# Kernel tuning notes

Hardware: AMD Instinct MI355X
Metric: run time of the kernel (lower is better)

Reference implementation:

```python
import jax, jax.numpy as jnp
import numpy as np

N, E, F, DE, G, C = 50000, 800000, 64, 32, 512, 2
EPS = 1e-5


def setup_inputs() -> dict:
    key = jax.random.key(0)
    ks = jax.random.split(key, 12)
    Z = 2 * F + DE  # CGConv concat dim [x_i, x_j, edge_attr]
    inp = {
        "x": jax.random.normal(ks[0], (N, F), dtype=jnp.float32),
        "edge_index": jax.random.randint(ks[1], (2, E), 0, N, dtype=jnp.int32),
        "edge_attr": jax.random.normal(ks[2], (E, DE), dtype=jnp.float32),
        "batch": jnp.sort(jax.random.randint(ks[3], (N,), 0, G, dtype=jnp.int32)),
        # CGConv lin_f / lin_s : (2F+De) -> F, with bias
        "Wf": jax.random.normal(ks[4], (Z, F), dtype=jnp.float32) * 0.05,
        "bf": jnp.zeros((F,), dtype=jnp.float32),
        "Ws": jax.random.normal(ks[5], (Z, F), dtype=jnp.float32) * 0.05,
        "bs": jnp.zeros((F,), dtype=jnp.float32),
        # CGConv internal BatchNorm (training-mode batch stats)
        "bn_w": jnp.ones((F,), dtype=jnp.float32),
        "bn_b": jnp.zeros((F,), dtype=jnp.float32),
        # PyG LayerNorm (graph mode, batch=None -> whole-tensor stats)
        "ln_w": jnp.ones((F,), dtype=jnp.float32),
        "ln_b": jnp.zeros((F,), dtype=jnp.float32),
        # final linear (2F -> C) and output LayerNorm
        "Wl": jax.random.normal(ks[6], (2 * F, C), dtype=jnp.float32) * 0.05,
        "bl": jnp.zeros((C,), dtype=jnp.float32),
        "ln4_w": jnp.ones((C,), dtype=jnp.float32),
        "ln4_b": jnp.zeros((C,), dtype=jnp.float32),
    }
    return inp


def _pyg_layernorm(x, w, b):
    # torch_geometric.nn.LayerNorm, mode='graph', batch=None: whole-tensor stats
    xc = x - jnp.mean(x)
    out = xc / (jnp.sqrt(jnp.mean(xc * xc)) + EPS)
    return out * w + b


def reference(x, edge_index, edge_attr, batch, Wf, bf, Ws, bs, bn_w, bn_b,
              ln_w, ln_b, Wl, bl, ln4_w, ln4_b):
    src = edge_index[0]  # x_j (source)
    dst = edge_index[1]  # x_i (target / aggregation index)

    # CGConv message: sigmoid(lin_f(z)) * softplus(lin_s(z)), z=[x_i,x_j,e]
    z = jnp.concatenate([x[dst], x[src], edge_attr], axis=1)  # [E, 2F+De]
    msg = jax.nn.sigmoid(z @ Wf + bf) * jax.nn.softplus(z @ Ws + bs)  # [E,F]

    # scatter-add aggregation to target nodes
    agg = jax.ops.segment_sum(msg, dst, num_segments=N)  # [N,F]

    # CGConv batch_norm=True (training-mode batch statistics over nodes)
    mu = jnp.mean(agg, axis=0)
    var = jnp.mean((agg - mu) ** 2, axis=0)
    agg = (agg - mu) / jnp.sqrt(var + EPS) * bn_w + bn_b

    # residual
    h = agg + x

    # LayerNorm + softplus
    h = jax.nn.softplus(_pyg_layernorm(h, ln_w, ln_b))

    # global mean / add pooling over graphs
    add_pool = jax.ops.segment_sum(h, batch, num_segments=G)  # [G,F]
    counts = jax.ops.segment_sum(jnp.ones((N,), h.dtype), batch, num_segments=G)
    mean_pool = add_pool / jnp.maximum(counts, 1.0)[:, None]

    g = jnp.concatenate([mean_pool, add_pool], axis=1)  # [G, 2F]
    out = g @ Wl + bl  # [G, C]
    out = _pyg_layernorm(out, ln4_w, ln4_b)
    return out
```

## Files before the change

### kernel.cpp

```cpp
#include <hip/hip_runtime.h>
#include <math.h>

#define EPSF 1e-5f

typedef short bf16x8 __attribute__((ext_vector_type(8)));
typedef float f32x4 __attribute__((ext_vector_type(4)));

static __device__ __forceinline__ unsigned short f2bf(float x) {
  unsigned u = __float_as_uint(x);
  unsigned r = (u + 0x7FFFu + ((u >> 16) & 1u)) >> 16;
  return (unsigned short)r;
}

static __device__ __forceinline__ float msgv(float F, float S) {
  float sig = __builtin_amdgcn_rcpf(1.0f + __expf(-F));
  float sp = fmaxf(S, 0.f) + __logf(1.0f + __expf(-fabsf(S)));
  return sig * sp;
}

__global__ __launch_bounds__(256) void prep_kernel(
    const float* __restrict__ x, const float* __restrict__ Wf,
    const float* __restrict__ Ws, const int* __restrict__ ei,
    unsigned short* __restrict__ xbf, unsigned short* __restrict__ Bfrag,
    unsigned short* __restrict__ Bfrag2, int* __restrict__ deg, int NCV,
    int total8, int E) {
  const int b = blockIdx.x, t = threadIdx.x;
  if (b < NCV) {
    int i = b * 256 + t;
    if (i < total8) {
      float4 a = ((const float4*)x)[i * 2];
      float4 c = ((const float4*)x)[i * 2 + 1];
      unsigned short o[8];
      o[0] = f2bf(a.x); o[1] = f2bf(a.y); o[2] = f2bf(a.z); o[3] = f2bf(a.w);
      o[4] = f2bf(c.x); o[5] = f2bf(c.y); o[6] = f2bf(c.z); o[7] = f2bf(c.w);
      ((uint4*)xbf)[i] = *(uint4*)o;
    }
  } else if (b < NCV + 6) {
    int g2 = (b - NCV) * 256 + t;
    if (g2 < 1536) {
      const int ks = g2 >> 9, t8 = (g2 >> 6) & 7, l = g2 & 63;
      const int q = l & 15, g = l >> 4;
      const float* W = (t8 < 4) ? Wf : Ws;
      const int col = (t8 & 3) * 16 + q;
      unsigned short out[8];
#pragma unroll
      for (int i = 0; i < 8; ++i) {
        int kk = ks * 32 + g * 8 + i;
        int wr = (kk < 32) ? (128 + kk) : (32 + kk);
        out[i] = f2bf(W[(size_t)wr * 64 + col]);
      }
      *(uint4*)&Bfrag[((size_t)(ks * 8 + t8) * 64 + l) * 8] = *(uint4*)out;
    }
  } else if (b < NCV + 10) {
    int g2 = (b - NCV - 6) * 256 + t;
    if (g2 < 1024) {
      const int ks = g2 >> 9, t8 = (g2 >> 6) & 7, l = g2 & 63;
      const int q = l & 15, g = l >> 4;
      const float* W = (t8 < 4) ? Wf : Ws;
      const int col = (t8 & 3) * 16 + q;
      unsigned short out[8];
#pragma unroll
      for (int i = 0; i < 8; ++i) {
        int kk = ks * 32 + g * 8 + i;
        out[i] = f2bf(W[(size_t)kk * 64 + col]);
      }
      *(uint4*)&Bfrag2[((size_t)(ks * 8 + t8) * 64 + l) * 8] = *(uint4*)out;
    }
  } else {
    int i = (b - NCV - 10) * 256 + t;
    if (i < E) atomicAdd(&deg[ei[E + i]], 1);
  }
}

__global__ __launch_bounds__(256, 4) void node_mfma(
    const unsigned short* __restrict__ xbf,
    const unsigned short* __restrict__ Bfrag2, const float* __restrict__ bf_,
    const float* __restrict__ bs_, unsigned* __restrict__ Pd, int N) {
  __shared__ __align__(16) short Bsh[16][64][8];
  for (int i = threadIdx.x; i < 1024; i += 256)
    ((uint4*)Bsh)[i] = ((const uint4*)Bfrag2)[i];
  __syncthreads();
  const int lane = threadIdx.x & 63, w = threadIdx.x >> 6;
  const int q = lane & 15, g = lane >> 4;
  const int row0 = blockIdx.x * 64;
  const float bfv = bf_[w * 16 + q], bsv = bs_[w * 16 + q];
  f32x4 accf[4], accs[4];
#pragma unroll
  for (int mt = 0; mt < 4; ++mt) {
    accf[mt] = (f32x4){0.f, 0.f, 0.f, 0.f};
    accs[mt] = (f32x4){0.f, 0.f, 0.f, 0.f};
  }
#pragma unroll
  for (int ks = 0; ks < 2; ++ks) {
    const bf16x8 Bfr = *(const bf16x8*)&Bsh[ks * 8 + w][lane][0];
    const bf16x8 Bsr = *(const bf16x8*)&Bsh[ks * 8 + 4 + w][lane][0];
#pragma unroll
    for (int mt = 0; mt < 4; ++mt) {
      int row = min(row0 + mt * 16 + q, N - 1);
      const bf16x8 a = *(const bf16x8*)(xbf + (size_t)row * 64 + ks * 32 + g * 8);
      accf[mt] = __builtin_amdgcn_mfma_f32_16x16x32_bf16(a, Bfr, accf[mt], 0, 0, 0);
      accs[mt] = __builtin_amdgcn_mfma_f32_16x16x32_bf16(a, Bsr, accs[mt], 0, 0, 0);
    }
  }
#pragma unroll
  for (int mt = 0; mt < 4; ++mt) {
#pragma unroll
    for (int r = 0; r < 4; ++r) {
      int row = row0 + mt * 16 + g * 4 + r;
      if (row < N) {
        unsigned u = ((unsigned)f2bf(accf[mt][r] + bfv) << 16) |
                     (unsigned)f2bf(accs[mt][r] + bsv);
        Pd[(size_t)row * 64 + w * 16 + q] = u;
      }
    }
  }
}

__global__ __launch_bounds__(256) void scan_a(const int* __restrict__ deg,
                                              int* __restrict__ bsum, int N) {
  const int idx = blockIdx.x * 256 + threadIdx.x;
  int v = (idx < N) ? deg[idx] : 0;
#pragma unroll
  for (int o = 32; o > 0; o >>= 1) v += __shfl_down(v, o);
  __shared__ int ws4[4];
  if ((threadIdx.x & 63) == 0) ws4[threadIdx.x >> 6] = v;
  __syncthreads();
  if (threadIdx.x == 0) bsum[blockIdx.x] = ws4[0] + ws4[1] + ws4[2] + ws4[3];
}

__global__ __launch_bounds__(256) void scan_b(const int* __restrict__ bsum,
                                              int* __restrict__ bpre, int NB) {
  const int t = threadIdx.x;
  const int lane = t & 63, w = t >> 6;
  int v = (t < NB) ? bsum[t] : 0;
  int sc = v;
#pragma unroll
  for (int o = 1; o < 64; o <<= 1) {
    int u = __shfl_up(sc, o);
    if (lane >= o) sc += u;
  }
  __shared__ int wsum[4];
  if (lane == 63) wsum[w] = sc;
  __syncthreads();
  int add = 0;
#pragma unroll
  for (int k = 0; k < 4; ++k) add += (k < w) ? wsum[k] : 0;
  bpre[t] = (sc - v) + add;
}

__global__ __launch_bounds__(256) void scan_c(const int* __restrict__ deg,
                                              const int* __restrict__ bpre,
                                              int* __restrict__ cursor, int N) {
  const int t = threadIdx.x;
  const int lane = t & 63, w = t >> 6;
  const int idx = blockIdx.x * 256 + t;
  int d = (idx < N) ? deg[idx] : 0;
  int sc = d;
#pragma unroll
  for (int o = 1; o < 64; o <<= 1) {
    int u = __shfl_up(sc, o);
    if (lane >= o) sc += u;
  }
  __shared__ int wsum[4];
  if (lane == 63) wsum[w] = sc;
  __syncthreads();
  int add = bpre[blockIdx.x];
#pragma unroll
  for (int k = 0; k < 4; ++k) add += (k < w) ? wsum[k] : 0;
  if (idx < N) cursor[idx] = add + (sc - d);
}

__global__ void scatter_kernel(const int* __restrict__ ei,
                               int* __restrict__ cursor,
                               int4* __restrict__ epair4, int E) {
  int i = blockIdx.x * 256 + threadIdx.x;
  if (i >= E) return;
  int dst = ei[E + i];
  int pos = atomicAdd(&cursor[dst], 1);
  epair4[pos] = make_int4(i, ei[i], dst, 0);
}

__global__ __launch_bounds__(256, 4) void edge_fused(
    const int4* __restrict__ epair4, const float* __restrict__ eattr,
    const unsigned short* __restrict__ xbf,
    const unsigned short* __restrict__ Bfrag, const unsigned* __restrict__ Pd,
    float* __restrict__ agg, int T16, int N, int E) {
  __shared__ __align__(16) short Bsh[24][64][8];
  for (int i = threadIdx.x; i < 1536; i += 256)
    ((uint4*)Bsh)[i] = ((const uint4*)Bfrag)[i];
  __syncthreads();

  const int lane = threadIdx.x & 63, w = threadIdx.x >> 6;
  const int q = lane & 15, g = lane >> 4;

  const int nB = gridDim.x;
  const int cb = (blockIdx.x & 7) * (nB >> 3) + (blockIdx.x >> 3);
  const int q8 = T16 / nB, r8 = T16 - q8 * nB;
  const int t0 = cb * q8 + min(cb, r8);
  const int t1 = t0 + q8 + (cb < r8 ? 1 : 0);

  int t = t0 + w;
  if (t >= t1) return;

  int4 p = epair4[(size_t)t * 16 + q];
  unsigned exi = min((unsigned)p.x, (unsigned)(E - 1));
  float4 eA = *(const float4*)(eattr + (size_t)exi * 32 + g * 8);
  float4 eB = *(const float4*)(eattr + (size_t)exi * 32 + g * 8 + 4);
  unsigned su = min((unsigned)p.y, (unsigned)(N - 1));
  bf16x8 aX0 = *(const bf16x8*)(xbf + (size_t)su * 64 + g * 8);
  bf16x8 aX1 = *(const bf16x8*)(xbf + (size_t)su * 64 + 32 + g * 8);

  while (true) {
    const int tn = t + 4;
    const bool more = (tn < t1);
    int4 pn = p;
    float4 eAn = eA, eBn = eB;
    bf16x8 aX0n = aX0, aX1n = aX1;
    if (more) {
      pn = epair4[(size_t)tn * 16 + q];
      unsigned exn = min((unsigned)pn.x, (unsigned)(E - 1));
      eAn = *(const float4*)(eattr + (size_t)exn * 32 + g * 8);
      eBn = *(const float4*)(eattr + (size_t)exn * 32 + g * 8 + 4);
      unsigned sn = min((unsigned)pn.y, (unsigned)(N - 1));
      aX0n = *(const bf16x8*)(xbf + (size_t)sn * 64 + g * 8);
      aX1n = *(const bf16x8*)(xbf + (size_t)sn * 64 + 32 + g * 8);
    }

    bf16x8 aE;
    aE[0] = (short)f2bf(eA.x); aE[1] = (short)f2bf(eA.y);
    aE[2] = (short)f2bf(eA.z); aE[3] = (short)f2bf(eA.w);
    aE[4] = (short)f2bf(eB.x); aE[5] = (short)f2bf(eB.y);
    aE[6] = (short)f2bf(eB.z); aE[7] = (short)f2bf(eB.w);

    f32x4 accf[4], accs[4];
#pragma unroll
    for (int nt = 0; nt < 4; ++nt) {
      f32x4 z = {0.f, 0.f, 0.f, 0.f};
      accf[nt] = __builtin_amdgcn_mfma_f32_16x16x32_bf16(
          aE, *(const bf16x8*)&Bsh[nt][lane][0], z, 0, 0, 0);
      accf[nt] = __builtin_amdgcn_mfma_f32_16x16x32_bf16(
          aX0, *(const bf16x8*)&Bsh[8 + nt][lane][0], accf[nt], 0, 0, 0);
      accf[nt] = __builtin_amdgcn_mfma_f32_16x16x32_bf16(
          aX1, *(const bf16x8*)&Bsh[16 + nt][lane][0], accf[nt], 0, 0, 0);
      f32x4 z2 = {0.f, 0.f, 0.f, 0.f};
      accs[nt] = __builtin_amdgcn_mfma_f32_16x16x32_bf16(
          aE, *(const bf16x8*)&Bsh[4 + nt][lane][0], z2, 0, 0, 0);
      accs[nt] = __builtin_amdgcn_mfma_f32_16x16x32_bf16(
          aX0, *(const bf16x8*)&Bsh[12 + nt][lane][0], accs[nt], 0, 0, 0);
      accs[nt] = __builtin_amdgcn_mfma_f32_16x16x32_bf16(
          aX1, *(const bf16x8*)&Bsh[20 + nt][lane][0], accs[nt], 0, 0, 0);
    }

    const int dA = __shfl(p.z, 0);
    const int dB = __shfl(p.z, 15);
    if (dA == dB) {
      const unsigned du = min((unsigned)dA, (unsigned)(N - 1));
      float tot0, tot1, tot2, tot3;
#pragma unroll
      for (int cg = 0; cg < 4; ++cg) {
        unsigned pdw = Pd[(size_t)du * 64 + cg * 16 + q];
        float pf = __uint_as_float(pdw & 0xFFFF0000u);
        float ps = __uint_as_float(pdw << 16);
        float s = msgv(accf[cg][0] + pf, accs[cg][0] + ps) +
                  msgv(accf[cg][1] + pf, accs[cg][1] + ps) +
                  msgv(accf[cg][2] + pf, accs[cg][2] + ps) +
                  msgv(accf[cg][3] + pf, accs[cg][3] + ps);
        s += __shfl_xor(s, 16);
        s += __shfl_xor(s, 32);
        if (cg == 0) tot0 = s;
        else if (cg == 1) tot1 = s;
        else if (cg == 2) tot2 = s;
        else tot3 = s;
      }
      float v = (g == 0) ? tot0 : (g == 1) ? tot1 : (g == 2) ? tot2 : tot3;
      if ((unsigned)dA < (unsigned)N)
        atomicAdd(&agg[(size_t)dA * 64 + g * 16 + q], v);
    } else {
      const int d0 = __shfl(p.z, g * 4);
      const int d1 = __shfl(p.z, g * 4 + 1);
      const int d2 = __shfl(p.z, g * 4 + 2);
      const int d3 = __shfl(p.z, g * 4 + 3);
#pragma unroll
      for (int cg = 0; cg < 4; ++cg) {
        const int feat = cg * 16 + q;
        const unsigned* Pr = Pd + feat;
        unsigned dc = (unsigned)d0;
        unsigned dl = min(dc, (unsigned)(N - 1));
        unsigned pdw = Pr[(size_t)dl * 64];
        float pf = __uint_as_float(pdw & 0xFFFF0000u);
        float ps = __uint_as_float(pdw << 16);
        float a_ = msgv(accf[cg][0] + pf, accs[cg][0] + ps);
#define STEP(DR, RIDX)                                                        \
  {                                                                           \
    unsigned dr = (unsigned)(DR);                                             \
    if (dr != dc) {                                                           \
      if (dc < (unsigned)N) atomicAdd(&agg[(size_t)dc * 64 + feat], a_);      \
      dc = dr; dl = min(dc, (unsigned)(N - 1));                               \
      pdw = Pr[(size_t)dl * 64];                                              \
      pf = __uint_as_float(pdw & 0xFFFF0000u);                                \
      ps = __uint_as_float(pdw << 16);                                        \
      a_ = 0.f;                                                               \
    }                                                                         \
    a_ += msgv(accf[cg][RIDX] + pf, accs[cg][RIDX] + ps);                     \
  }
        STEP(d1, 1)
        STEP(d2, 2)
        STEP(d3, 3)
#undef STEP
        if (dc < (unsigned)N) atomicAdd(&agg[(size_t)dc * 64 + feat], a_);
      }
    }

    if (!more) break;
    p = pn; eA = eAn; eB = eBn; aX0 = aX0n; aX1 = aX1n; t = tn;
  }
}

__global__ __launch_bounds__(256) void stats_kernel(
    const float* __restrict__ agg, const float* __restrict__ x,
    float* __restrict__ stats, int N) {
  const int f = threadIdx.x & 63;
  const int sub = threadIdx.x >> 6;
  float sa = 0, sa2 = 0, sx = 0, sx2 = 0, sax = 0;
  for (int r = blockIdx.x * 4 + sub; r < N; r += gridDim.x * 4) {
    float a = agg[(size_t)r * 64 + f];
    float xv = x[(size_t)r * 64 + f];
    sa += a; sa2 += a * a; sx += xv; sx2 += xv * xv; sax += a * xv;
  }
  __shared__ float lds[4][5][64];
  lds[sub][0][f] = sa; lds[sub][1][f] = sa2; lds[sub][2][f] = sx;
  lds[sub][3][f] = sx2; lds[sub][4][f] = sax;
  __syncthreads();
  if (sub == 0) {
#pragma unroll
    for (int i = 0; i < 5; ++i) {
      float v = lds[0][i][f] + lds[1][i][f] + lds[2][i][f] + lds[3][i][f];
      atomicAdd(&stats[i * 64 + f], v);
    }
  }
}

__global__ __launch_bounds__(256) void node_finish(
    const float* __restrict__ stats, const float* __restrict__ bn_w,
    const float* __restrict__ bn_b, const float* __restrict__ agg,
    const float* __restrict__ x, const int* __restrict__ batch,
    const float* __restrict__ ln_w, const float* __restrict__ ln_b,
    float* __restrict__ add_pool, float* __restrict__ counts, int N,
    int chunk) {
  const int f = threadIdx.x & 63;
  const int sub = threadIdx.x >> 6;
  const float Nf = (float)N;
  const float invN = 1.0f / Nf;
  float Sa = stats[f], Sa2 = stats[64 + f], Sx = stats[128 + f],
        Sx2 = stats[192 + f], Sax = stats[256 + f];
  float mu = Sa * invN;
  float var = Sa2 * invN - mu * mu;
  const float alpha = bn_w[f] / sqrtf(var + EPSF);
  const float beta = bn_b[f] - mu * alpha;
  float Sh = alpha * Sa + Nf * beta + Sx;
  float Sh2 = alpha * alpha * Sa2 + Sx2 + Nf * beta * beta +
              2.f * alpha * Sax + 2.f * alpha * beta * Sa + 2.f * beta * Sx;
#pragma unroll
  for (int o = 32; o > 0; o >>= 1) {
    Sh += __shfl_xor(Sh, o);
    Sh2 += __shfl_xor(Sh2, o);
  }
  const float cnt = Nf * 64.0f;
  const float mean = Sh / cnt;
  const float msq = Sh2 / cnt - mean * mean;
  const float rden = 1.0f / (sqrtf(fmaxf(msq, 0.f)) + EPSF);
  const float lw = ln_w[f] * rden;
  const float lb = ln_b[f];

  const int r0 = blockIdx.x * chunk;
  const int r1 = min(N, r0 + chunk);
  float acc = 0.f, cacc = 0.f;
  int curg = -1;
  for (int r = r0 + sub; r < r1; r += 4) {
    int g = batch[r];
    if (g != curg) {
      if (curg >= 0) {
        atomicAdd(&add_pool[(size_t)curg * 64 + f], acc);
        if (f == 0) atomicAdd(&counts[curg], cacc);
      }
      curg = g; acc = 0.f; cacc = 0.f;
    }
    float h = fmaf(alpha, agg[(size_t)r * 64 + f], beta) + x[(size_t)r * 64 + f];
    float v = (h - mean) * lw + lb;
    float sp = fmaxf(v, 0.f) + __logf(1.0f + __expf(-fabsf(v)));
    acc += sp; cacc += 1.f;
  }
  if (curg >= 0) {
    atomicAdd(&add_pool[(size_t)curg * 64 + f], acc);
    if (f == 0) atomicAdd(&counts[curg], cacc);
  }
}

__global__ __launch_bounds__(1024) void graph_out(
    const float* __restrict__ add_pool, const float* __restrict__ counts,
    const float* __restrict__ Wl, const float* __restrict__ bl,
    const float* __restrict__ w4, const float* __restrict__ b4,
    float* __restrict__ out, int G) {
  const int t = threadIdx.x;
  const int g = t >> 1, c = t & 1;
  float cnt = fmaxf(counts[g], 1.0f);
  float inv = 1.0f / cnt;
  const float4* ap4 = (const float4*)(add_pool + (size_t)g * 64);
  const float4* W4 = (const float4*)Wl;
  float v = bl[c];
#pragma unroll 4
  for (int k4 = 0; k4 < 16; ++k4) {
    float4 a4 = ap4[k4];
    float4 wa = W4[k4 * 2];
    float4 wb = W4[k4 * 2 + 1];
    float4 wc = W4[32 + k4 * 2];
    float4 wd = W4[32 + k4 * 2 + 1];
    float m0 = c ? wa.y : wa.x, m1 = c ? wa.w : wa.z;
    float m2 = c ? wb.y : wb.x, m3 = c ? wb.w : wb.z;
    float a0 = c ? wc.y : wc.x, a1 = c ? wc.w : wc.z;
    float a2 = c ? wd.y : wd.x, a3 = c ? wd.w : wd.z;
    v = fmaf(a4.x, fmaf(m0, inv, a0), v);
    v = fmaf(a4.y, fmaf(m1, inv, a1), v);
    v = fmaf(a4.z, fmaf(m2, inv, a2), v);
    v = fmaf(a4.w, fmaf(m3, inv, a3), v);
  }

  __shared__ float red[16];
  __shared__ float bc[2];
  float sum = v;
#pragma unroll
  for (int o = 32; o > 0; o >>= 1) sum += __shfl_down(sum, o);
  if ((t & 63) == 0) red[t >> 6] = sum;
  __syncthreads();
  if (t == 0) {
    float tot = 0;
#pragma unroll
    for (int i = 0; i < 16; ++i) tot += red[i];
    bc[0] = tot * (1.0f / 1024.0f);
  }
  __syncthreads();
  const float mean = bc[0];
  const float xc = v - mean;
  float sq = xc * xc;
  __syncthreads();
#pragma unroll
  for (int o = 32; o > 0; o >>= 1) sq += __shfl_down(sq, o);
  if ((t & 63) == 0) red[t >> 6] = sq;
  __syncthreads();
  if (t == 0) {
    float tot = 0;
#pragma unroll
    for (int i = 0; i < 16; ++i) tot += red[i];
    bc[1] = 1.0f / (sqrtf(tot * (1.0f / 1024.0f)) + EPSF);
  }
  __syncthreads();
  out[t] = xc * bc[1] * w4[c] + b4[c];
}

extern "C" void kernel_launch(void* const* d_in, const int* in_sizes, int n_in,
                              void* d_out, int out_size, void* d_ws,
                              size_t ws_size, hipStream_t stream) {
  const float* x = (const float*)d_in[0];
  const int* ei = (const int*)d_in[1];
  const float* eattr = (const float*)d_in[2];
  const int* batch = (const int*)d_in[3];
  const float* Wf = (const float*)d_in[4];
  const float* bf = (const float*)d_in[5];
  const float* Ws = (const float*)d_in[6];
  const float* bs = (const float*)d_in[7];
  const float* bn_w = (const float*)d_in[8];
  const float* bn_b = (const float*)d_in[9];
  const float* ln_w = (const float*)d_in[10];
  const float* ln_b = (const float*)d_in[11];
  const float* Wl = (const float*)d_in[12];
  const float* bl = (const float*)d_in[13];
  const float* w4 = (const float*)d_in[14];
  const float* b4 = (const float*)d_in[15];

  const int N = in_sizes[0] / 64;
  const int E = in_sizes[2] / 32;
  const int G = 512;
  const int NB = (N + 255) / 256;
  const int T16 = (E + 15) / 16;
  const int NCV = (N * 8 + 255) / 256;
  const int NH = (E + 255) / 256;

  float* ws = (float*)d_ws;
  float* agg = ws;
  float* stats = agg + (size_t)N * 64;
  float* add_pool = stats + 320;
  float* counts = add_pool + (size_t)G * 64;
  int* deg = (int*)(counts + G);
  int* cursor = deg + N;
  int* bsum = cursor + N;
  int* bpre = bsum + 256;
  unsigned short* Bfrag = (unsigned short*)(bpre + 256);
  unsigned short* Bfrag2 = Bfrag + 12288;
  unsigned short* xbf = Bfrag2 + 8192;
  unsigned* Pd = (unsigned*)(xbf + (size_t)N * 64);
  int4* epair4 = (int4*)(Pd + (size_t)N * 64);

  size_t zeroFloats = (size_t)N * 64 + 320 + (size_t)G * 64 + G + N;
  hipMemsetAsync(agg, 0, zeroFloats * sizeof(float), stream);
  const int padE = T16 * 16 - E;
  if (padE > 0) hipMemsetAsync(epair4 + E, 0xFF, (size_t)padE * 16, stream);

  prep_kernel<<<NCV + 10 + NH, 256, 0, stream>>>(x, Wf, Ws, ei, xbf, Bfrag,
                                                 Bfrag2, deg, NCV, N * 8, E);
  node_mfma<<<(N + 63) / 64, 256, 0, stream>>>(xbf, Bfrag2, bf, bs, Pd, N);
  scan_a<<<NB, 256, 0, stream>>>(deg, bsum, N);
  scan_b<<<1, 256, 0, stream>>>(bsum, bpre, NB);
  scan_c<<<NB, 256, 0, stream>>>(deg, bpre, cursor, N);
  scatter_kernel<<<NH, 256, 0, stream>>>(ei, cursor, epair4, E);
  edge_fused<<<1024, 256, 0, stream>>>(epair4, eattr, xbf, Bfrag, Pd, agg, T16,
                                       N, E);
  stats_kernel<<<512, 256, 0, stream>>>(agg, x, stats, N);
  const int chunk = (N + 511) / 512;
  node_finish<<<512, 256, 0, stream>>>(stats, bn_w, bn_b, agg, x, batch, ln_w,
                                       ln_b, add_pool, counts, N, chunk);
  graph_out<<<1, 1024, 0, stream>>>(add_pool, counts, Wl, bl, w4, b4,
                                    (float*)d_out, G);
}
```

Measured before the change: 371.0 us.

## Accumulate edge messages in an LDS window and pack edge index pairs

The edge kernel now accumulates messages for destination nodes that fall in a small per-block window (starting at the block's first destination) into shared memory. It then flushes each touched row to global memory with one atomic per feature, instead of issuing global atomics for every tile. Destinations outside the window still go straight to global atomics. The sorted edge records also shrink from int4 to int2 by packing source and destination into 16-bit halves. This cuts gather bandwidth but only works while N is below 65536, and the extra shared memory may lower occupancy.

```diff
diff --git a/kernel.cpp b/kernel.cpp
--- a/kernel.cpp
+++ b/kernel.cpp
@@ -2,6 +2,7 @@
 #include <math.h>
 
 #define EPSF 1e-5f
+#define WIN 56
 
 typedef short bf16x8 __attribute__((ext_vector_type(8)));
 typedef float f32x4 __attribute__((ext_vector_type(4)));
@@ -172,22 +173,26 @@
 
 __global__ void scatter_kernel(const int* __restrict__ ei,
                                int* __restrict__ cursor,
-                               int4* __restrict__ epair4, int E) {
+                               int2* __restrict__ epair2, int E) {
   int i = blockIdx.x * 256 + threadIdx.x;
   if (i >= E) return;
   int dst = ei[E + i];
   int pos = atomicAdd(&cursor[dst], 1);
-  epair4[pos] = make_int4(i, ei[i], dst, 0);
+  epair2[pos] = make_int2(i, ei[i] | (dst << 16));
 }
 
 __global__ __launch_bounds__(256, 4) void edge_fused(
-    const int4* __restrict__ epair4, const float* __restrict__ eattr,
+    const int2* __restrict__ epair2, const float* __restrict__ eattr,
     const unsigned short* __restrict__ xbf,
     const unsigned short* __restrict__ Bfrag, const unsigned* __restrict__ Pd,
     float* __restrict__ agg, int T16, int N, int E) {
   __shared__ __align__(16) short Bsh[24][64][8];
+  __shared__ float msum[WIN][64];
+  __shared__ int touched[WIN];
   for (int i = threadIdx.x; i < 1536; i += 256)
     ((uint4*)Bsh)[i] = ((const uint4*)Bfrag)[i];
+  for (int i = threadIdx.x; i < WIN * 64; i += 256) ((float*)msum)[i] = 0.f;
+  for (int i = threadIdx.x; i < WIN; i += 256) touched[i] = 0;
   __syncthreads();
 
   const int lane = threadIdx.x & 63, w = threadIdx.x >> 6;
@@ -199,102 +204,113 @@
   const int t0 = cb * q8 + min(cb, r8);
   const int t1 = t0 + q8 + (cb < r8 ? 1 : 0);
 
+  const int dstBase = (int)(((unsigned)epair2[(size_t)t0 * 16].y) >> 16);
+
+#define FLUSH(DC, FEAT, VAL)                                                  \
+  {                                                                           \
+    int _idx = (int)(DC)-dstBase;                                             \
+    if ((unsigned)_idx < (unsigned)WIN) {                                     \
+      atomicAdd(&msum[_idx][FEAT], (VAL));                                    \
+      touched[_idx] = 1;                                                      \
+    } else if ((DC) < (unsigned)N) {                                          \
+      atomicAdd(&agg[(size_t)(DC)*64 + (FEAT)], (VAL));                       \
+    }                                                                         \
+  }
+
   int t = t0 + w;
-  if (t >= t1) return;
-
-  int4 p = epair4[(size_t)t * 16 + q];
-  unsigned exi = min((unsigned)p.x, (unsigned)(E - 1));
-  float4 eA = *(const float4*)(eattr + (size_t)exi * 32 + g * 8);
-  float4 eB = *(const float4*)(eattr + (size_t)exi * 32 + g * 8 + 4);
-  unsigned su = min((unsigned)p.y, (unsigned)(N - 1));
-  bf16x8 aX0 = *(const bf16x8*)(xbf + (size_t)su * 64 + g * 8);
-  bf16x8 aX1 = *(const bf16x8*)(xbf + (size_t)su * 64 + 32 + g * 8);
-
-  while (true) {
-    const int tn = t + 4;
-    const bool more = (tn < t1);
-    int4 pn = p;
-    float4 eAn = eA, eBn = eB;
-    bf16x8 aX0n = aX0, aX1n = aX1;
-    if (more) {
-      pn = epair4[(size_t)tn * 16 + q];
-      unsigned exn = min((unsigned)pn.x, (unsigned)(E - 1));
-      eAn = *(const float4*)(eattr + (size_t)exn * 32 + g * 8);
-      eBn = *(const float4*)(eattr + (size_t)exn * 32 + g * 8 + 4);
-      unsigned sn = min((unsigned)pn.y, (unsigned)(N - 1));
-      aX0n = *(const bf16x8*)(xbf + (size_t)sn * 64 + g * 8);
-      aX1n = *(const bf16x8*)(xbf + (size_t)sn * 64 + 32 + g * 8);
-    }
-
-    bf16x8 aE;
-    aE[0] = (short)f2bf(eA.x); aE[1] = (short)f2bf(eA.y);
-    aE[2] = (short)f2bf(eA.z); aE[3] = (short)f2bf(eA.w);
-    aE[4] = (short)f2bf(eB.x); aE[5] = (short)f2bf(eB.y);
-    aE[6] = (short)f2bf(eB.z); aE[7] = (short)f2bf(eB.w);
-
-    f32x4 accf[4], accs[4];
-#pragma unroll
-    for (int nt = 0; nt < 4; ++nt) {
-      f32x4 z = {0.f, 0.f, 0.f, 0.f};
-      accf[nt] = __builtin_amdgcn_mfma_f32_16x16x32_bf16(
-          aE, *(const bf16x8*)&Bsh[nt][lane][0], z, 0, 0, 0);
-      accf[nt] = __builtin_amdgcn_mfma_f32_16x16x32_bf16(
-          aX0, *(const bf16x8*)&Bsh[8 + nt][lane][0], accf[nt], 0, 0, 0);
-      accf[nt] = __builtin_amdgcn_mfma_f32_16x16x32_bf16(
-          aX1, *(const bf16x8*)&Bsh[16 + nt][lane][0], accf[nt], 0, 0, 0);
-      f32x4 z2 = {0.f, 0.f, 0.f, 0.f};
-      accs[nt] = __builtin_amdgcn_mfma_f32_16x16x32_bf16(
-          aE, *(const bf16x8*)&Bsh[4 + nt][lane][0], z2, 0, 0, 0);
-      accs[nt] = __builtin_amdgcn_mfma_f32_16x16x32_bf16(
-          aX0, *(const bf16x8*)&Bsh[12 + nt][lane][0], accs[nt], 0, 0, 0);
-      accs[nt] = __builtin_amdgcn_mfma_f32_16x16x32_bf16(
-          aX1, *(const bf16x8*)&Bsh[20 + nt][lane][0], accs[nt], 0, 0, 0);
-    }
-
-    const int dA = __shfl(p.z, 0);
-    const int dB = __shfl(p.z, 15);
-    if (dA == dB) {
-      const unsigned du = min((unsigned)dA, (unsigned)(N - 1));
-      float tot0, tot1, tot2, tot3;
-#pragma unroll
-      for (int cg = 0; cg < 4; ++cg) {
-        unsigned pdw = Pd[(size_t)du * 64 + cg * 16 + q];
-        float pf = __uint_as_float(pdw & 0xFFFF0000u);
-        float ps = __uint_as_float(pdw << 16);
-        float s = msgv(accf[cg][0] + pf, accs[cg][0] + ps) +
-                  msgv(accf[cg][1] + pf, accs[cg][1] + ps) +
-                  msgv(accf[cg][2] + pf, accs[cg][2] + ps) +
-                  msgv(accf[cg][3] + pf, accs[cg][3] + ps);
-        s += __shfl_xor(s, 16);
-        s += __shfl_xor(s, 32);
-        if (cg == 0) tot0 = s;
-        else if (cg == 1) tot1 = s;
-        else if (cg == 2) tot2 = s;
-        else tot3 = s;
-      }
-      float v = (g == 0) ? tot0 : (g == 1) ? tot1 : (g == 2) ? tot2 : tot3;
-      if ((unsigned)dA < (unsigned)N)
-        atomicAdd(&agg[(size_t)dA * 64 + g * 16 + q], v);
-    } else {
-      const int d0 = __shfl(p.z, g * 4);
-      const int d1 = __shfl(p.z, g * 4 + 1);
-      const int d2 = __shfl(p.z, g * 4 + 2);
-      const int d3 = __shfl(p.z, g * 4 + 3);
-#pragma unroll
-      for (int cg = 0; cg < 4; ++cg) {
-        const int feat = cg * 16 + q;
-        const unsigned* Pr = Pd + feat;
-        unsigned dc = (unsigned)d0;
-        unsigned dl = min(dc, (unsigned)(N - 1));
-        unsigned pdw = Pr[(size_t)dl * 64];
-        float pf = __uint_as_float(pdw & 0xFFFF0000u);
-        float ps = __uint_as_float(pdw << 16);
-        float a_ = msgv(accf[cg][0] + pf, accs[cg][0] + ps);
+  if (t < t1) {
+    int2 p = epair2[(size_t)t * 16 + q];
+    unsigned exi = min((unsigned)p.x, (unsigned)(E - 1));
+    float4 eA = *(const float4*)(eattr + (size_t)exi * 32 + g * 8);
+    float4 eB = *(const float4*)(eattr + (size_t)exi * 32 + g * 8 + 4);
+    unsigned su = min((unsigned)p.y & 0xFFFFu, (unsigned)(N - 1));
+    bf16x8 aX0 = *(const bf16x8*)(xbf + (size_t)su * 64 + g * 8);
+    bf16x8 aX1 = *(const bf16x8*)(xbf + (size_t)su * 64 + 32 + g * 8);
+
+    while (true) {
+      const int tn = t + 4;
+      const bool more = (tn < t1);
+      int2 pn = p;
+      float4 eAn = eA, eBn = eB;
+      bf16x8 aX0n = aX0, aX1n = aX1;
+      if (more) {
+        pn = epair2[(size_t)tn * 16 + q];
+        unsigned exn = min((unsigned)pn.x, (unsigned)(E - 1));
+        eAn = *(const float4*)(eattr + (size_t)exn * 32 + g * 8);
+        eBn = *(const float4*)(eattr + (size_t)exn * 32 + g * 8 + 4);
+        unsigned sn = min((unsigned)pn.y & 0xFFFFu, (unsigned)(N - 1));
+        aX0n = *(const bf16x8*)(xbf + (size_t)sn * 64 + g * 8);
+        aX1n = *(const bf16x8*)(xbf + (size_t)sn * 64 + 32 + g * 8);
+      }
+
+      bf16x8 aE;
+      aE[0] = (short)f2bf(eA.x); aE[1] = (short)f2bf(eA.y);
+      aE[2] = (short)f2bf(eA.z); aE[3] = (short)f2bf(eA.w);
+      aE[4] = (short)f2bf(eB.x); aE[5] = (short)f2bf(eB.y);
+      aE[6] = (short)f2bf(eB.z); aE[7] = (short)f2bf(eB.w);
+
+      f32x4 accf[4], accs[4];
+#pragma unroll
+      for (int nt = 0; nt < 4; ++nt) {
+        f32x4 z = {0.f, 0.f, 0.f, 0.f};
+        accf[nt] = __builtin_amdgcn_mfma_f32_16x16x32_bf16(
+            aE, *(const bf16x8*)&Bsh[nt][lane][0], z, 0, 0, 0);
+        accf[nt] = __builtin_amdgcn_mfma_f32_16x16x32_bf16(
+            aX0, *(const bf16x8*)&Bsh[8 + nt][lane][0], accf[nt], 0, 0, 0);
+        accf[nt] = __builtin_amdgcn_mfma_f32_16x16x32_bf16(
+            aX1, *(const bf16x8*)&Bsh[16 + nt][lane][0], accf[nt], 0, 0, 0);
+        f32x4 z2 = {0.f, 0.f, 0.f, 0.f};
+        accs[nt] = __builtin_amdgcn_mfma_f32_16x16x32_bf16(
+            aE, *(const bf16x8*)&Bsh[4 + nt][lane][0], z2, 0, 0, 0);
+        accs[nt] = __builtin_amdgcn_mfma_f32_16x16x32_bf16(
+            aX0, *(const bf16x8*)&Bsh[12 + nt][lane][0], accs[nt], 0, 0, 0);
+        accs[nt] = __builtin_amdgcn_mfma_f32_16x16x32_bf16(
+            aX1, *(const bf16x8*)&Bsh[20 + nt][lane][0], accs[nt], 0, 0, 0);
+      }
+
+      const unsigned dA = ((unsigned)__shfl(p.y, 0)) >> 16;
+      const unsigned dB = ((unsigned)__shfl(p.y, 15)) >> 16;
+      if (dA == dB) {
+        const unsigned du = min(dA, (unsigned)(N - 1));
+        float tot0, tot1, tot2, tot3;
+#pragma unroll
+        for (int cg = 0; cg < 4; ++cg) {
+          unsigned pdw = Pd[(size_t)du * 64 + cg * 16 + q];
+          float pf = __uint_as_float(pdw & 0xFFFF0000u);
+          float ps = __uint_as_float(pdw << 16);
+          float s = msgv(accf[cg][0] + pf, accs[cg][0] + ps) +
+                    msgv(accf[cg][1] + pf, accs[cg][1] + ps) +
+                    msgv(accf[cg][2] + pf, accs[cg][2] + ps) +
+                    msgv(accf[cg][3] + pf, accs[cg][3] + ps);
+          s += __shfl_xor(s, 16);
+          s += __shfl_xor(s, 32);
+          if (cg == 0) tot0 = s;
+          else if (cg == 1) tot1 = s;
+          else if (cg == 2) tot2 = s;
+          else tot3 = s;
+        }
+        float v = (g == 0) ? tot0 : (g == 1) ? tot1 : (g == 2) ? tot2 : tot3;
+        FLUSH(dA, g * 16 + q, v);
+      } else {
+        const unsigned d0 = ((unsigned)__shfl(p.y, g * 4)) >> 16;
+        const unsigned d1 = ((unsigned)__shfl(p.y, g * 4 + 1)) >> 16;
+        const unsigned d2 = ((unsigned)__shfl(p.y, g * 4 + 2)) >> 16;
+        const unsigned d3 = ((unsigned)__shfl(p.y, g * 4 + 3)) >> 16;
+#pragma unroll
+        for (int cg = 0; cg < 4; ++cg) {
+          const int feat = cg * 16 + q;
+          const unsigned* Pr = Pd + feat;
+          unsigned dc = d0;
+          unsigned dl = min(dc, (unsigned)(N - 1));
+          unsigned pdw = Pr[(size_t)dl * 64];
+          float pf = __uint_as_float(pdw & 0xFFFF0000u);
+          float ps = __uint_as_float(pdw << 16);
+          float a_ = msgv(accf[cg][0] + pf, accs[cg][0] + ps);
 #define STEP(DR, RIDX)                                                        \
   {                                                                           \
-    unsigned dr = (unsigned)(DR);                                             \
+    unsigned dr = (DR);                                                       \
     if (dr != dc) {                                                           \
-      if (dc < (unsigned)N) atomicAdd(&agg[(size_t)dc * 64 + feat], a_);      \
+      FLUSH(dc, feat, a_);                                                    \
       dc = dr; dl = min(dc, (unsigned)(N - 1));                               \
       pdw = Pr[(size_t)dl * 64];                                              \
       pf = __uint_as_float(pdw & 0xFFFF0000u);                                \
@@ -303,17 +319,27 @@
     }                                                                         \
     a_ += msgv(accf[cg][RIDX] + pf, accs[cg][RIDX] + ps);                     \
   }
-        STEP(d1, 1)
-        STEP(d2, 2)
-        STEP(d3, 3)
+          STEP(d1, 1)
+          STEP(d2, 2)
+          STEP(d3, 3)
 #undef STEP
-        if (dc < (unsigned)N) atomicAdd(&agg[(size_t)dc * 64 + feat], a_);
-      }
-    }
-
-    if (!more) break;
-    p = pn; eA = eAn; eB = eBn; aX0 = aX0n; aX1 = aX1n; t = tn;
-  }
+          FLUSH(dc, feat, a_);
+        }
+      }
+
+      if (!more) break;
+      p = pn; eA = eAn; eB = eBn; aX0 = aX0n; aX1 = aX1n; t = tn;
+    }
+  }
+
+  __syncthreads();
+  for (int n = w; n < WIN; n += 4) {
+    if (touched[n]) {
+      unsigned dn = (unsigned)(dstBase + n);
+      if (dn < (unsigned)N) atomicAdd(&agg[(size_t)dn * 64 + lane], msum[n][lane]);
+    }
+  }
+#undef FLUSH
 }
 
 __global__ __launch_bounds__(256) void stats_kernel(
@@ -498,12 +524,12 @@
   unsigned short* Bfrag2 = Bfrag + 12288;
   unsigned short* xbf = Bfrag2 + 8192;
   unsigned* Pd = (unsigned*)(xbf + (size_t)N * 64);
-  int4* epair4 = (int4*)(Pd + (size_t)N * 64);
+  int2* epair2 = (int2*)(Pd + (size_t)N * 64);
 
   size_t zeroFloats = (size_t)N * 64 + 320 + (size_t)G * 64 + G + N;
   hipMemsetAsync(agg, 0, zeroFloats * sizeof(float), stream);
   const int padE = T16 * 16 - E;
-  if (padE > 0) hipMemsetAsync(epair4 + E, 0xFF, (size_t)padE * 16, stream);
+  if (padE > 0) hipMemsetAsync(epair2 + E, 0xFF, (size_t)padE * 8, stream);
 
   prep_kernel<<<NCV + 10 + NH, 256, 0, stream>>>(x, Wf, Ws, ei, xbf, Bfrag,
                                                  Bfrag2, deg, NCV, N * 8, E);
@@ -511,8 +537,8 @@
   scan_a<<<NB, 256, 0, stream>>>(deg, bsum, N);
   scan_b<<<1, 256, 0, stream>>>(bsum, bpre, NB);
   scan_c<<<NB, 256, 0, stream>>>(deg, bpre, cursor, N);
-  scatter_kernel<<<NH, 256, 0, stream>>>(ei, cursor, epair4, E);
-  edge_fused<<<1024, 256, 0, stream>>>(epair4, eattr, xbf, Bfrag, Pd, agg, T16,
+  scatter_kernel<<<NH, 256, 0, stream>>>(ei, cursor, epair2, E);
+  edge_fused<<<1024, 256, 0, stream>>>(epair2, eattr, xbf, Bfrag, Pd, agg, T16,
                                        N, E);
   stats_kernel<<<512, 256, 0, stream>>>(agg, x, stats, N);
   const int chunk = (N + 511) / 512;
```

Result: faster. 345.5 us (-6.9%).
